# Performance work log

Hardware: AMD Instinct MI355X
Metric: run time of the kernel (lower is better)

Reference implementation:

```python
import jax, jax.numpy as jnp
import numpy as np

VOCAB = 128
HIDDEN = 256


def setup_inputs() -> dict:
    key = jax.random.key(0)
    ks = jax.random.split(key, 8)
    B, S = 64, 2048
    # first feature channel: event-type ids stored as floats (module does .long())
    ev = jax.random.randint(ks[0], (B, S, 1), 0, VOCAB).astype(jnp.float32)
    num = jax.random.normal(ks[1], (B, S, 7), dtype=jnp.float32)
    X = jnp.concatenate([ev, num], axis=-1)  # [B,S,8]
    emb_table = jax.random.normal(ks[2], (VOCAB, 124), dtype=jnp.float32) * 0.1
    W_num = jax.random.normal(ks[3], (4, 7), dtype=jnp.float32) * 0.3
    b_num = jnp.zeros((4,), dtype=jnp.float32)
    W_conv = jax.random.normal(ks[4], (3 * HIDDEN, 128), dtype=jnp.float32) * 0.08
    b_conv = jnp.zeros((3 * HIDDEN,), dtype=jnp.float32)
    W_out = jax.random.normal(ks[5], (1, HIDDEN), dtype=jnp.float32) * 0.06
    b_out = jnp.zeros((1,), dtype=jnp.float32)
    return {"X": X, "emb_table": emb_table, "W_num": W_num, "b_num": b_num,
            "W_conv": W_conv, "b_conv": b_conv, "W_out": W_out, "b_out": b_out}


def reference(X, emb_table, W_num, b_num, W_conv, b_conv, W_out, b_out):
    # X: [B,S,8] -- channel 0 = event id, channels 1: = numeric attrs
    event = jax.lax.stop_gradient(X[:, :, 0]).astype(jnp.int32)   # [B,S]
    numeric = X[:, :, 1:]                                          # [B,S,7]
    emb = emb_table[event]                                         # [B,S,124]
    tn = numeric @ W_num.T + b_num                                 # [B,S,4]
    comb = jnp.concatenate([emb, tn], axis=-1)                     # [B,S,128]
    # Conv1d with kernel_size=1 == pointwise linear to 3*hidden gates
    gates = comb @ W_conv.T + b_conv                               # [B,S,3H]
    gates = jnp.transpose(gates, (1, 0, 2))                        # [S,B,3H]
    Z, F, O = jnp.split(gates, 3, axis=2)
    Z = jnp.tanh(Z)
    F = jax.nn.sigmoid(F)
    O = jax.nn.sigmoid(O)

    def step(h, zfo):
        z, f, o = zfo
        h = f * h + (1.0 - f) * z
        return h, o * h

    h0 = jnp.zeros(Z.shape[1:], dtype=Z.dtype)                     # [B,H]
    _, hs = jax.lax.scan(step, h0, (Z, F, O))                      # hs: [S,B,H]
    final_rep = hs[-1]                                             # [B,H]
    # dropout is identity at inference (dropout=0 / eval)
    return final_rep @ W_out.T + b_out                             # [B,1]
```

## Files before the change

kernel.cpp:

```cpp
#include <hip/hip_runtime.h>


typedef float f32x2 __attribute__((ext_vector_type(2)));
typedef float f32x4 __attribute__((ext_vector_type(4)));

#define NB 64
#define NS 2048
#define NH 256
#define CHUNKS 32
#define STEPS (NS / CHUNKS)
#define LOG2E 1.4426950408889634f
#define PAD 129

__global__ __launch_bounds__(256) void precompute_kernel(
    const float* __restrict__ X,
    const float* __restrict__ emb,
    const float* __restrict__ Wn,
    const float* __restrict__ bn,
    const float* __restrict__ Wc,
    const float* __restrict__ bc,
    f32x2* __restrict__ G2,
    float* __restrict__ Go,
    f32x2* __restrict__ Wg2,
    float* __restrict__ Wgo,
    int*   __restrict__ Eoff)
{
    __shared__ float M[124 * PAD];
    const int tid = threadIdx.x;
    const int blk = blockIdx.x;

    if (blk < 64) {
        {
            const int e = tid >> 1, half = tid & 1;
            const f32x4* er4 = (const f32x4*)(emb + (size_t)e * 124);
            #pragma unroll
            for (int i = 0; i < 16; ++i) {
                const int idx = half * 16 + i;
                if (idx < 31) {
                    const f32x4 v = er4[idx];
                    const int k0 = idx * 4;
                    M[(k0 + 0) * PAD + e] = v.x;
                    M[(k0 + 1) * PAD + e] = v.y;
                    M[(k0 + 2) * PAD + e] = v.z;
                    M[(k0 + 3) * PAD + e] = v.w;
                }
            }
        }
        __syncthreads();

        const int e = tid & 127;
        const int s = tid >> 7;
        const int j0 = blk * 4 + s * 2;

        float bnv[4];
        #pragma unroll
        for (int m = 0; m < 4; ++m) bnv[m] = bn[m];

        float acc[2][3] = {{0.f,0.f,0.f},{0.f,0.f,0.f}};
        const f32x4* wz4[2]; const f32x4* wf4[2]; const f32x4* wo4[2];
        #pragma unroll
        for (int i = 0; i < 2; ++i) {
            wz4[i] = (const f32x4*)(Wc + (size_t)(j0 + i) * 128);
            wf4[i] = (const f32x4*)(Wc + (size_t)(j0 + i + 256) * 128);
            wo4[i] = (const f32x4*)(Wc + (size_t)(j0 + i + 512) * 128);
        }

        for (int kb = 0; kb < 31; ++kb) {
            f32x4 w[2][3];
            #pragma unroll
            for (int i = 0; i < 2; ++i) {
                w[i][0] = wz4[i][kb];
                w[i][1] = wf4[i][kb];
                w[i][2] = wo4[i][kb];
            }
            #pragma unroll
            for (int u = 0; u < 4; ++u) {
                const float mv = M[(kb * 4 + u) * PAD + e];
                #pragma unroll
                for (int i = 0; i < 2; ++i) {
                    acc[i][0] = fmaf(w[i][0][u], mv, acc[i][0]);
                    acc[i][1] = fmaf(w[i][1][u], mv, acc[i][1]);
                    acc[i][2] = fmaf(w[i][2][u], mv, acc[i][2]);
                }
            }
        }

        #pragma unroll
        for (int i = 0; i < 2; ++i) {
            const int j = j0 + i;
            float az = acc[i][0] + bc[j];
            float af = acc[i][1] + bc[j + 256];
            float ao = acc[i][2] + bc[j + 512];
            const f32x4 tz = wz4[i][31];
            const f32x4 tf = wf4[i][31];
            const f32x4 to = wo4[i][31];
            #pragma unroll
            for (int m = 0; m < 4; ++m) {
                az = fmaf(tz[m], bnv[m], az);
                af = fmaf(tf[m], bnv[m], af);
                ao = fmaf(to[m], bnv[m], ao);
            }
            G2[(size_t)e * NH + j] = (f32x2){az * (-2.0f * LOG2E), af * (-LOG2E)};
            Go[(size_t)e * NH + j] = ao * (-LOG2E);
        }
    } else if (blk == 64) {
        const int j = tid;
        #pragma unroll
        for (int n = 0; n < 7; ++n) {
            float sz = 0.0f, sf = 0.0f, so = 0.0f;
            #pragma unroll
            for (int m = 0; m < 4; ++m) {
                const float wnm = Wn[m * 7 + n];
                sz = fmaf(Wc[(size_t)j * 128 + 124 + m], wnm, sz);
                sf = fmaf(Wc[(size_t)(j + 256) * 128 + 124 + m], wnm, sf);
                so = fmaf(Wc[(size_t)(j + 512) * 128 + 124 + m], wnm, so);
            }
            Wg2[n * NH + j] = (f32x2){sz * (-2.0f * LOG2E), sf * (-LOG2E)};
            Wgo[n * NH + j] = so * (-LOG2E);
        }
    } else {
        const int base = (blk - 65) * 1024 + tid;
        #pragma unroll
        for (int u = 0; u < 4; ++u) {
            const int idx = base + u * 256;
            Eoff[idx] = ((int)X[(size_t)idx * 8]) << 11;
        }
    }
}

__global__ __launch_bounds__(256) void scan_kernel(
    const float* __restrict__ X,
    const int* __restrict__ Eoff,
    const f32x2* __restrict__ G2,
    const float* __restrict__ Go,
    const f32x2* __restrict__ Wg2,
    const float* __restrict__ Wgo,
    float* __restrict__ AB,
    float* __restrict__ Olast)
{
    const int b = blockIdx.x;
    const int c = blockIdx.y;
    const int j = threadIdx.x;

    const int*   __restrict__ ep = Eoff + b * NS + c * STEPS;
    const float* __restrict__ xp = X + ((size_t)b * NS + (size_t)c * STEPS) * 8;
    const char*  __restrict__ g2b = (const char*)G2;
    const char*  __restrict__ gob = (const char*)Go;
    const int j8 = j * 8;

    f32x2 w2[7];
    #pragma unroll
    for (int n = 0; n < 7; ++n) w2[n] = Wg2[n * NH + j];

    float A = 1.0f, Bv = 0.0f;
    #pragma unroll 8
    for (int t = 0; t < STEPS; ++t) {
        const int eo = ep[t];
        f32x2 g2 = *(const f32x2*)(g2b + eo + j8);
        #pragma unroll
        for (int n = 0; n < 7; ++n) {
            const float xn = xp[t * 8 + 1 + n];
            g2 = __builtin_elementwise_fma(w2[n], (f32x2){xn, xn}, g2);
        }
        const float ez = __builtin_amdgcn_exp2f(g2.x);
        const float ef = __builtin_amdgcn_exp2f(g2.y);
        const float z = fmaf(2.0f, __builtin_amdgcn_rcpf(1.0f + ez), -1.0f);
        const float f = __builtin_amdgcn_rcpf(1.0f + ef);
        A *= f;
        Bv = fmaf(f, Bv - z, z);
    }

    AB[(((size_t)c * NB + b) * 2 + 0) * NH + j] = A;
    AB[(((size_t)c * NB + b) * 2 + 1) * NH + j] = Bv;

    if (c == CHUNKS - 1) {
        const int t = STEPS - 1;
        const int eo = ep[t];
        float go = *(const float*)(gob + (eo >> 1) + j * 4);
        #pragma unroll
        for (int n = 0; n < 7; ++n) {
            go = fmaf(Wgo[n * NH + j], xp[t * 8 + 1 + n], go);
        }
        Olast[b * NH + j] = __builtin_amdgcn_rcpf(1.0f + __builtin_amdgcn_exp2f(go));
    }
}

__global__ __launch_bounds__(256) void combine_kernel(
    const float* __restrict__ AB,
    const float* __restrict__ Olast,
    const float* __restrict__ Wout,
    const float* __restrict__ bout,
    float* __restrict__ out)
{
    const int b = blockIdx.x;
    const int j = threadIdx.x;

    float h = 0.0f;
    #pragma unroll 8
    for (int c = 0; c < CHUNKS; ++c) {
        const float A  = AB[(((size_t)c * NB + b) * 2 + 0) * NH + j];
        const float Bv = AB[(((size_t)c * NB + b) * 2 + 1) * NH + j];
        h = fmaf(A, h, Bv);
    }
    float v = Olast[b * NH + j] * h * Wout[j];

    #pragma unroll
    for (int off = 32; off > 0; off >>= 1) v += __shfl_down(v, off);
    __shared__ float red[4];
    if ((j & 63) == 0) red[j >> 6] = v;
    __syncthreads();
    if (j == 0) out[b] = red[0] + red[1] + red[2] + red[3] + bout[0];
}

extern "C" void kernel_launch(void* const* d_in, const int* in_sizes, int n_in,
                              void* d_out, int out_size, void* d_ws, size_t ws_size,
                              hipStream_t stream) {
    const float* X    = (const float*)d_in[0];
    const float* emb  = (const float*)d_in[1];
    const float* Wn   = (const float*)d_in[2];
    const float* bn   = (const float*)d_in[3];
    const float* Wc   = (const float*)d_in[4];
    const float* bc   = (const float*)d_in[5];
    const float* Wout = (const float*)d_in[6];
    const float* bout = (const float*)d_in[7];
    float* out = (float*)d_out;

    f32x2* G2  = (f32x2*)d_ws;
    float* Go  = (float*)(G2 + 128 * NH);
    f32x2* Wg2 = (f32x2*)(Go + 128 * NH);
    float* Wgo = (float*)(Wg2 + 7 * NH);
    float* AB  = Wgo + 7 * NH;
    float* Ol  = AB + (size_t)CHUNKS * NB * 2 * NH;
    int*   Eo  = (int*)(Ol + NB * NH);

    precompute_kernel<<<193, 256, 0, stream>>>(X, emb, Wn, bn, Wc, bc,
                                               G2, Go, Wg2, Wgo, Eo);
    dim3 grid(NB, CHUNKS);
    scan_kernel<<<grid, 256, 0, stream>>>(X, Eo, G2, Go, Wg2, Wgo, AB, Ol);
    combine_kernel<<<NB, 256, 0, stream>>>(AB, Ol, Wout, bout, out);
}
```

Before: 40.91 us.

## Process two hidden channels per thread with vector loads and prefetch in scan

```diff
diff --git a/kernel.cpp b/kernel.cpp
--- a/kernel.cpp
+++ b/kernel.cpp
@@ -12,6 +12,8 @@
 #define LOG2E 1.4426950408889634f
 #define PAD 129
 
+static __device__ __forceinline__ f32x4 splat4(float v) { return (f32x4){v, v, v, v}; }
+
 __global__ __launch_bounds__(256) void precompute_kernel(
     const float* __restrict__ X,
     const float* __restrict__ emb,
@@ -19,11 +21,11 @@
     const float* __restrict__ bn,
     const float* __restrict__ Wc,
     const float* __restrict__ bc,
-    f32x2* __restrict__ G2,
+    f32x4* __restrict__ G4,
     float* __restrict__ Go,
-    f32x2* __restrict__ Wg2,
-    float* __restrict__ Wgo,
-    int*   __restrict__ Eoff)
+    f32x4* __restrict__ Wg4,
+    f32x2* __restrict__ Wgo2,
+    float* __restrict__ Xp)
 {
     __shared__ float M[124 * PAD];
     const int tid = threadIdx.x;
@@ -51,6 +53,7 @@
         const int e = tid & 127;
         const int s = tid >> 7;
         const int j0 = blk * 4 + s * 2;
+        const int p  = blk * 2 + s;
 
         float bnv[4];
         #pragma unroll
@@ -85,6 +88,7 @@
             }
         }
 
+        float azv[2], afv[2], aov[2];
         #pragma unroll
         for (int i = 0; i < 2; ++i) {
             const int j = j0 + i;
@@ -100,88 +104,129 @@
                 af = fmaf(tf[m], bnv[m], af);
                 ao = fmaf(to[m], bnv[m], ao);
             }
-            G2[(size_t)e * NH + j] = (f32x2){az * (-2.0f * LOG2E), af * (-LOG2E)};
-            Go[(size_t)e * NH + j] = ao * (-LOG2E);
-        }
+            azv[i] = az; afv[i] = af; aov[i] = ao;
+        }
+        G4[(size_t)e * 128 + p] = (f32x4){azv[0] * (-2.0f * LOG2E), afv[0] * (-LOG2E),
+                                          azv[1] * (-2.0f * LOG2E), afv[1] * (-LOG2E)};
+        Go[(size_t)e * NH + j0]     = aov[0] * (-LOG2E);
+        Go[(size_t)e * NH + j0 + 1] = aov[1] * (-LOG2E);
     } else if (blk == 64) {
-        const int j = tid;
-        #pragma unroll
-        for (int n = 0; n < 7; ++n) {
-            float sz = 0.0f, sf = 0.0f, so = 0.0f;
-            #pragma unroll
-            for (int m = 0; m < 4; ++m) {
-                const float wnm = Wn[m * 7 + n];
-                sz = fmaf(Wc[(size_t)j * 128 + 124 + m], wnm, sz);
-                sf = fmaf(Wc[(size_t)(j + 256) * 128 + 124 + m], wnm, sf);
-                so = fmaf(Wc[(size_t)(j + 512) * 128 + 124 + m], wnm, so);
-            }
-            Wg2[n * NH + j] = (f32x2){sz * (-2.0f * LOG2E), sf * (-LOG2E)};
-            Wgo[n * NH + j] = so * (-LOG2E);
+        if (tid < 128) {
+            #pragma unroll
+            for (int n = 0; n < 7; ++n) {
+                float s0[3] = {0.f,0.f,0.f}, s1[3] = {0.f,0.f,0.f};
+                #pragma unroll
+                for (int m = 0; m < 4; ++m) {
+                    const float wnm = Wn[m * 7 + n];
+                    const int j0 = 2 * tid, j1 = 2 * tid + 1;
+                    s0[0] = fmaf(Wc[(size_t)j0 * 128 + 124 + m], wnm, s0[0]);
+                    s0[1] = fmaf(Wc[(size_t)(j0 + 256) * 128 + 124 + m], wnm, s0[1]);
+                    s0[2] = fmaf(Wc[(size_t)(j0 + 512) * 128 + 124 + m], wnm, s0[2]);
+                    s1[0] = fmaf(Wc[(size_t)j1 * 128 + 124 + m], wnm, s1[0]);
+                    s1[1] = fmaf(Wc[(size_t)(j1 + 256) * 128 + 124 + m], wnm, s1[1]);
+                    s1[2] = fmaf(Wc[(size_t)(j1 + 512) * 128 + 124 + m], wnm, s1[2]);
+                }
+                Wg4[n * 128 + tid]  = (f32x4){s0[0] * (-2.0f * LOG2E), s0[1] * (-LOG2E),
+                                              s1[0] * (-2.0f * LOG2E), s1[1] * (-LOG2E)};
+                Wgo2[n * 128 + tid] = (f32x2){s0[2] * (-LOG2E), s1[2] * (-LOG2E)};
+            }
+        } else if (tid < 136) {
+            Xp[(size_t)NB * NS * 8 + (tid - 128)] = 0.0f;
         }
     } else {
+        const f32x4* X4 = (const f32x4*)X;
+        f32x4* Xp4 = (f32x4*)Xp;
         const int base = (blk - 65) * 1024 + tid;
         #pragma unroll
         for (int u = 0; u < 4; ++u) {
             const int idx = base + u * 256;
-            Eoff[idx] = ((int)X[(size_t)idx * 8]) << 11;
-        }
-    }
-}
-
-__global__ __launch_bounds__(256) void scan_kernel(
-    const float* __restrict__ X,
-    const int* __restrict__ Eoff,
-    const f32x2* __restrict__ G2,
+            f32x4 xa = X4[(size_t)idx * 2];
+            const f32x4 xb = X4[(size_t)idx * 2 + 1];
+            xa.x = __int_as_float(((int)xa.x) << 11);
+            Xp4[(size_t)idx * 2]     = xa;
+            Xp4[(size_t)idx * 2 + 1] = xb;
+        }
+    }
+}
+
+__global__ __launch_bounds__(128) void scan_kernel(
+    const float* __restrict__ Xp,
+    const f32x4* __restrict__ G4,
     const float* __restrict__ Go,
-    const f32x2* __restrict__ Wg2,
-    const float* __restrict__ Wgo,
+    const f32x4* __restrict__ Wg4,
+    const f32x2* __restrict__ Wgo2,
     float* __restrict__ AB,
     float* __restrict__ Olast)
 {
     const int b = blockIdx.x;
     const int c = blockIdx.y;
-    const int j = threadIdx.x;
-
-    const int*   __restrict__ ep = Eoff + b * NS + c * STEPS;
-    const float* __restrict__ xp = X + ((size_t)b * NS + (size_t)c * STEPS) * 8;
-    const char*  __restrict__ g2b = (const char*)G2;
-    const char*  __restrict__ gob = (const char*)Go;
-    const int j8 = j * 8;
-
-    f32x2 w2[7];
+    const int tid = threadIdx.x;
+
+    const f32x4* __restrict__ xp =
+        (const f32x4*)(Xp + ((size_t)b * NS + (size_t)c * STEPS) * 8);
+    const char* __restrict__ g4b = (const char*)G4;
+    const int j16 = tid * 16;
+
+    f32x4 w4[7];
     #pragma unroll
-    for (int n = 0; n < 7; ++n) w2[n] = Wg2[n * NH + j];
-
-    float A = 1.0f, Bv = 0.0f;
-    #pragma unroll 8
+    for (int n = 0; n < 7; ++n) w4[n] = Wg4[n * 128 + tid];
+
+    f32x4 xa = xp[0], xb = xp[1];
+    f32x4 g = *(const f32x4*)(g4b + __float_as_int(xa.x) + j16);
+
+    float A0 = 1.f, B0 = 0.f, A1 = 1.f, B1 = 0.f;
+    #pragma unroll 4
     for (int t = 0; t < STEPS; ++t) {
-        const int eo = ep[t];
-        f32x2 g2 = *(const f32x2*)(g2b + eo + j8);
+        const f32x4 xa_n = xp[2 * t + 2];
+        const f32x4 xb_n = xp[2 * t + 3];
+        const f32x4 g_n = *(const f32x4*)(g4b + __float_as_int(xa_n.x) + j16);
+
+        f32x4 acc = g;
+        acc = __builtin_elementwise_fma(w4[0], splat4(xa.y), acc);
+        acc = __builtin_elementwise_fma(w4[1], splat4(xa.z), acc);
+        acc = __builtin_elementwise_fma(w4[2], splat4(xa.w), acc);
+        acc = __builtin_elementwise_fma(w4[3], splat4(xb.x), acc);
+        acc = __builtin_elementwise_fma(w4[4], splat4(xb.y), acc);
+        acc = __builtin_elementwise_fma(w4[5], splat4(xb.z), acc);
+        acc = __builtin_elementwise_fma(w4[6], splat4(xb.w), acc);
+
+        const float ez0 = __builtin_amdgcn_exp2f(acc.x);
+        const float ef0 = __builtin_amdgcn_exp2f(acc.y);
+        const float ez1 = __builtin_amdgcn_exp2f(acc.z);
+        const float ef1 = __builtin_amdgcn_exp2f(acc.w);
+        const float az0 = 1.f + ez0, af0 = 1.f + ef0;
+        const float az1 = 1.f + ez1, af1 = 1.f + ef1;
+        const float r0 = __builtin_amdgcn_rcpf(az0 * af0);
+        const float r1 = __builtin_amdgcn_rcpf(az1 * af1);
+        const float f0 = r0 * az0;
+        const float f1 = r1 * az1;
+        const float z0 = fmaf(2.f, r0 * af0, -1.f);
+        const float z1 = fmaf(2.f, r1 * af1, -1.f);
+
+        A0 *= f0; B0 = fmaf(f0, B0 - z0, z0);
+        A1 *= f1; B1 = fmaf(f1, B1 - z1, z1);
+
+        g = g_n; xa = xa_n; xb = xb_n;
+    }
+
+    *(f32x2*)(AB + (((size_t)c * NB + b) * 2 + 0) * NH + 2 * tid) = (f32x2){A0, A1};
+    *(f32x2*)(AB + (((size_t)c * NB + b) * 2 + 1) * NH + 2 * tid) = (f32x2){B0, B1};
+
+    if (c == CHUNKS - 1) {
+        const f32x4 la = xp[2 * (STEPS - 1)];
+        const f32x4 lb = xp[2 * (STEPS - 1) + 1];
+        const int eol = __float_as_int(la.x);
+        f32x2 go = *(const f32x2*)((const char*)Go + (eol >> 1) + tid * 8);
+        const float xs[7] = {la.y, la.z, la.w, lb.x, lb.y, lb.z, lb.w};
         #pragma unroll
         for (int n = 0; n < 7; ++n) {
-            const float xn = xp[t * 8 + 1 + n];
-            g2 = __builtin_elementwise_fma(w2[n], (f32x2){xn, xn}, g2);
-        }
-        const float ez = __builtin_amdgcn_exp2f(g2.x);
-        const float ef = __builtin_amdgcn_exp2f(g2.y);
-        const float z = fmaf(2.0f, __builtin_amdgcn_rcpf(1.0f + ez), -1.0f);
-        const float f = __builtin_amdgcn_rcpf(1.0f + ef);
-        A *= f;
-        Bv = fmaf(f, Bv - z, z);
-    }
-
-    AB[(((size_t)c * NB + b) * 2 + 0) * NH + j] = A;
-    AB[(((size_t)c * NB + b) * 2 + 1) * NH + j] = Bv;
-
-    if (c == CHUNKS - 1) {
-        const int t = STEPS - 1;
-        const int eo = ep[t];
-        float go = *(const float*)(gob + (eo >> 1) + j * 4);
-        #pragma unroll
-        for (int n = 0; n < 7; ++n) {
-            go = fmaf(Wgo[n * NH + j], xp[t * 8 + 1 + n], go);
-        }
-        Olast[b * NH + j] = __builtin_amdgcn_rcpf(1.0f + __builtin_amdgcn_exp2f(go));
+            const f32x2 wg = Wgo2[n * 128 + tid];
+            go.x = fmaf(wg.x, xs[n], go.x);
+            go.y = fmaf(wg.y, xs[n], go.y);
+        }
+        const float o0 = __builtin_amdgcn_rcpf(1.f + __builtin_amdgcn_exp2f(go.x));
+        const float o1 = __builtin_amdgcn_rcpf(1.f + __builtin_amdgcn_exp2f(go.y));
+        *(f32x2*)(Olast + b * NH + 2 * tid) = (f32x2){o0, o1};
     }
 }
 
@@ -225,17 +270,17 @@
     const float* bout = (const float*)d_in[7];
     float* out = (float*)d_out;
 
-    f32x2* G2  = (f32x2*)d_ws;
-    float* Go  = (float*)(G2 + 128 * NH);
-    f32x2* Wg2 = (f32x2*)(Go + 128 * NH);
-    float* Wgo = (float*)(Wg2 + 7 * NH);
-    float* AB  = Wgo + 7 * NH;
-    float* Ol  = AB + (size_t)CHUNKS * NB * 2 * NH;
-    int*   Eo  = (int*)(Ol + NB * NH);
+    f32x4* G4   = (f32x4*)d_ws;
+    float* Go   = (float*)(G4 + 128 * 128);
+    f32x4* Wg4  = (f32x4*)(Go + 128 * NH);
+    f32x2* Wgo2 = (f32x2*)(Wg4 + 7 * 128);
+    float* AB   = (float*)(Wgo2 + 7 * 128);
+    float* Ol   = AB + (size_t)CHUNKS * NB * 2 * NH;
+    float* Xp   = Ol + NB * NH;
 
     precompute_kernel<<<193, 256, 0, stream>>>(X, emb, Wn, bn, Wc, bc,
-                                               G2, Go, Wg2, Wgo, Eo);
+                                               G4, Go, Wg4, Wgo2, Xp);
     dim3 grid(NB, CHUNKS);
-    scan_kernel<<<grid, 256, 0, stream>>>(X, Eo, G2, Go, Wg2, Wgo, AB, Ol);
+    scan_kernel<<<grid, 128, 0, stream>>>(Xp, G4, Go, Wg4, Wgo2, AB, Ol);
     combine_kernel<<<NB, 256, 0, stream>>>(AB, Ol, Wout, bout, out);
 }
```

New measurement: 43.47 us. 1.06x slower.

## Pack event offset into X copy and software-pipeline scan loads

Applied to the files above, without the earlier changes.

```diff
diff --git a/kernel.cpp b/kernel.cpp
--- a/kernel.cpp
+++ b/kernel.cpp
@@ -23,7 +23,7 @@
     float* __restrict__ Go,
     f32x2* __restrict__ Wg2,
     float* __restrict__ Wgo,
-    int*   __restrict__ Eoff)
+    float* __restrict__ Xp)
 {
     __shared__ float M[124 * PAD];
     const int tid = threadIdx.x;
@@ -104,33 +104,43 @@
             Go[(size_t)e * NH + j] = ao * (-LOG2E);
         }
     } else if (blk == 64) {
-        const int j = tid;
-        #pragma unroll
-        for (int n = 0; n < 7; ++n) {
-            float sz = 0.0f, sf = 0.0f, so = 0.0f;
-            #pragma unroll
-            for (int m = 0; m < 4; ++m) {
-                const float wnm = Wn[m * 7 + n];
-                sz = fmaf(Wc[(size_t)j * 128 + 124 + m], wnm, sz);
-                sf = fmaf(Wc[(size_t)(j + 256) * 128 + 124 + m], wnm, sf);
-                so = fmaf(Wc[(size_t)(j + 512) * 128 + 124 + m], wnm, so);
-            }
-            Wg2[n * NH + j] = (f32x2){sz * (-2.0f * LOG2E), sf * (-LOG2E)};
-            Wgo[n * NH + j] = so * (-LOG2E);
+        if (tid < 256) {
+            const int j = tid;
+            #pragma unroll
+            for (int n = 0; n < 7; ++n) {
+                float sz = 0.0f, sf = 0.0f, so = 0.0f;
+                #pragma unroll
+                for (int m = 0; m < 4; ++m) {
+                    const float wnm = Wn[m * 7 + n];
+                    sz = fmaf(Wc[(size_t)j * 128 + 124 + m], wnm, sz);
+                    sf = fmaf(Wc[(size_t)(j + 256) * 128 + 124 + m], wnm, sf);
+                    so = fmaf(Wc[(size_t)(j + 512) * 128 + 124 + m], wnm, so);
+                }
+                Wg2[n * NH + j] = (f32x2){sz * (-2.0f * LOG2E), sf * (-LOG2E)};
+                Wgo[n * NH + j] = so * (-LOG2E);
+            }
+        }
+        if (tid < 32) {
+            Xp[(size_t)NB * NS * 8 + tid] = 0.0f;
         }
     } else {
+        const f32x4* X4 = (const f32x4*)X;
+        f32x4* Xp4 = (f32x4*)Xp;
         const int base = (blk - 65) * 1024 + tid;
         #pragma unroll
         for (int u = 0; u < 4; ++u) {
             const int idx = base + u * 256;
-            Eoff[idx] = ((int)X[(size_t)idx * 8]) << 11;
+            f32x4 xa = X4[(size_t)idx * 2];
+            const f32x4 xb = X4[(size_t)idx * 2 + 1];
+            xa.x = __int_as_float(((int)xa.x) << 11);
+            Xp4[(size_t)idx * 2]     = xa;
+            Xp4[(size_t)idx * 2 + 1] = xb;
         }
     }
 }
 
 __global__ __launch_bounds__(256) void scan_kernel(
-    const float* __restrict__ X,
-    const int* __restrict__ Eoff,
+    const float* __restrict__ Xp,
     const f32x2* __restrict__ G2,
     const float* __restrict__ Go,
     const f32x2* __restrict__ Wg2,
@@ -142,30 +152,49 @@
     const int c = blockIdx.y;
     const int j = threadIdx.x;
 
-    const int*   __restrict__ ep = Eoff + b * NS + c * STEPS;
-    const float* __restrict__ xp = X + ((size_t)b * NS + (size_t)c * STEPS) * 8;
-    const char*  __restrict__ g2b = (const char*)G2;
-    const char*  __restrict__ gob = (const char*)Go;
+    const f32x4* __restrict__ xp =
+        (const f32x4*)(Xp + ((size_t)b * NS + (size_t)c * STEPS) * 8);
+    const char* __restrict__ g2b = (const char*)G2;
     const int j8 = j * 8;
 
     f32x2 w2[7];
     #pragma unroll
     for (int n = 0; n < 7; ++n) w2[n] = Wg2[n * NH + j];
 
+    f32x4 ra[4], rb[4];
+    f32x2 gg[4];
+    ra[0] = xp[0]; rb[0] = xp[1];
+    ra[1] = xp[2]; rb[1] = xp[3];
+    ra[2] = xp[4]; rb[2] = xp[5];
+    gg[0] = *(const f32x2*)(g2b + (size_t)(unsigned)__float_as_int(ra[0].x) + j8);
+    gg[1] = *(const f32x2*)(g2b + (size_t)(unsigned)__float_as_int(ra[1].x) + j8);
+
     float A = 1.0f, Bv = 0.0f;
-    #pragma unroll 8
+    #pragma unroll 4
     for (int t = 0; t < STEPS; ++t) {
-        const int eo = ep[t];
-        f32x2 g2 = *(const f32x2*)(g2b + eo + j8);
-        #pragma unroll
-        for (int n = 0; n < 7; ++n) {
-            const float xn = xp[t * 8 + 1 + n];
-            g2 = __builtin_elementwise_fma(w2[n], (f32x2){xn, xn}, g2);
-        }
-        const float ez = __builtin_amdgcn_exp2f(g2.x);
-        const float ef = __builtin_amdgcn_exp2f(g2.y);
-        const float z = fmaf(2.0f, __builtin_amdgcn_rcpf(1.0f + ez), -1.0f);
-        const float f = __builtin_amdgcn_rcpf(1.0f + ef);
+        ra[(t + 3) & 3] = xp[2 * (t + 3)];
+        rb[(t + 3) & 3] = xp[2 * (t + 3) + 1];
+        gg[(t + 2) & 3] = *(const f32x2*)(
+            g2b + (size_t)(unsigned)__float_as_int(ra[(t + 2) & 3].x) + j8);
+
+        const f32x4 xa = ra[t & 3];
+        const f32x4 xb = rb[t & 3];
+        f32x2 g = gg[t & 3];
+        g = __builtin_elementwise_fma(w2[0], (f32x2){xa.y, xa.y}, g);
+        g = __builtin_elementwise_fma(w2[1], (f32x2){xa.z, xa.z}, g);
+        g = __builtin_elementwise_fma(w2[2], (f32x2){xa.w, xa.w}, g);
+        g = __builtin_elementwise_fma(w2[3], (f32x2){xb.x, xb.x}, g);
+        g = __builtin_elementwise_fma(w2[4], (f32x2){xb.y, xb.y}, g);
+        g = __builtin_elementwise_fma(w2[5], (f32x2){xb.z, xb.z}, g);
+        g = __builtin_elementwise_fma(w2[6], (f32x2){xb.w, xb.w}, g);
+
+        const float ez = __builtin_amdgcn_exp2f(g.x);
+        const float ef = __builtin_amdgcn_exp2f(g.y);
+        const float az = 1.0f + ez, af = 1.0f + ef;
+        const float r = __builtin_amdgcn_rcpf(az * af);
+        const float f = r * az;
+        const float z = fmaf(2.0f, r * af, -1.0f);
+
         A *= f;
         Bv = fmaf(f, Bv - z, z);
     }
@@ -174,12 +203,14 @@
     AB[(((size_t)c * NB + b) * 2 + 1) * NH + j] = Bv;
 
     if (c == CHUNKS - 1) {
-        const int t = STEPS - 1;
-        const int eo = ep[t];
-        float go = *(const float*)(gob + (eo >> 1) + j * 4);
+        const f32x4 la = xp[2 * (STEPS - 1)];
+        const f32x4 lb = xp[2 * (STEPS - 1) + 1];
+        const int eo = __float_as_int(la.x);
+        float go = *(const float*)((const char*)Go + ((size_t)(unsigned)eo >> 1) + j * 4);
+        const float xs[7] = {la.y, la.z, la.w, lb.x, lb.y, lb.z, lb.w};
         #pragma unroll
         for (int n = 0; n < 7; ++n) {
-            go = fmaf(Wgo[n * NH + j], xp[t * 8 + 1 + n], go);
+            go = fmaf(Wgo[n * NH + j], xs[n], go);
         }
         Olast[b * NH + j] = __builtin_amdgcn_rcpf(1.0f + __builtin_amdgcn_exp2f(go));
     }
@@ -231,11 +262,11 @@
     float* Wgo = (float*)(Wg2 + 7 * NH);
     float* AB  = Wgo + 7 * NH;
     float* Ol  = AB + (size_t)CHUNKS * NB * 2 * NH;
-    int*   Eo  = (int*)(Ol + NB * NH);
+    float* Xp  = Ol + NB * NH;
 
     precompute_kernel<<<193, 256, 0, stream>>>(X, emb, Wn, bn, Wc, bc,
-                                               G2, Go, Wg2, Wgo, Eo);
+                                               G2, Go, Wg2, Wgo, Xp);
     dim3 grid(NB, CHUNKS);
-    scan_kernel<<<grid, 256, 0, stream>>>(X, Eo, G2, Go, Wg2, Wgo, AB, Ol);
+    scan_kernel<<<grid, 256, 0, stream>>>(Xp, G2, Go, Wg2, Wgo, AB, Ol);
     combine_kernel<<<NB, 256, 0, stream>>>(AB, Ol, Wout, bout, out);
 }
```

After: 46.85 us. 14.5% more time.
